# Kernel tuning notes

Hardware: AMD Instinct MI355X
Metric: run time of the kernel (lower is better)

The kernel has to match this reference:

```python
import jax, jax.numpy as jnp
import numpy as np

B, T, N, D, H, NMASK = 8192, 2, 40, 64, 1, 3
EPS = 1e-5


def setup_inputs() -> dict:
    key = jax.random.key(0)
    ks = jax.random.split(key, 12)
    F = T * N * 2 * D  # flattened feature size fed to BatchNorm1d
    return {
        "x": jax.random.normal(ks[0], (B, N, D), jnp.float32),
        "masker": jax.random.uniform(ks[1], (T, NMASK, N, N), jnp.float32, -0.27, 0.27),  # xavier-like
        "ln_gamma": jnp.ones((N,), jnp.float32),
        "ln_beta": jnp.zeros((N,), jnp.float32),
        "gnn_w": jax.random.normal(ks[2], (1, T, H, 2 * D, D), jnp.float32) * 0.05,
        "gnn_b": jax.random.normal(ks[3], (T, H, N, D), jnp.float32) * 0.05,
        "bn_gamma": jnp.ones((H, F), jnp.float32),
        "bn_beta": jnp.zeros((H, F), jnp.float32),
        "bn_mean": jax.random.normal(ks[4], (H, F), jnp.float32) * 0.1,
        "bn_var": jax.random.uniform(ks[5], (H, F), jnp.float32, 0.5, 1.5),
        "gate_w": jax.random.normal(ks[6], (N * D, N), jnp.float32) * 0.02,
        "gate_b": jnp.zeros((N,), jnp.float32),
    }


def reference(x, masker, ln_gamma, ln_beta, gnn_w, gnn_b, bn_gamma, bn_beta, bn_mean, bn_var, gate_w, gate_b):
    b = x.shape[0]
    # broadcast input to towers: (B, T, N, D)
    h = jnp.broadcast_to(x[:, None], (b, T, N, D))
    # adjacency from product of mask matrices: (T, N, N)
    adj = jax.nn.relu(jnp.prod(masker, axis=1))
    mask = (adj != 0).astype(x.dtype)
    # LayerNorm(num_fields) applied on transposed adj == normalize over rows (axis -2)
    mu = adj.mean(axis=-2, keepdims=True)
    var = adj.var(axis=-2, keepdims=True)
    ln = (adj - mu) / jnp.sqrt(var + EPS) * ln_gamma[:, None] + ln_beta[:, None]
    x_masked = ln + (1.0 - mask) * (-1e9) + jnp.eye(N, dtype=x.dtype)
    # softmax over rows (dim=1 of (T,N,N)) then re-mask
    A = jax.nn.softmax(x_masked, axis=1) * mask  # (T, N, N)
    for idx in range(H):
        # nei[b,t,n,d] = sum_m h[b,t,m,d] * A[t,m,n]
        nei = jnp.einsum('btmd,tmn->btnd', h, A)
        hc = jnp.concatenate([h, nei], axis=-1)  # (B,T,N,2D)
        flat = hc.reshape(b, -1)
        flat = (flat - bn_mean[idx]) / jnp.sqrt(bn_var[idx] + EPS) * bn_gamma[idx] + bn_beta[idx]
        hc = flat.reshape(b, T, N, 2 * D)
        # per-tower transform: (B,T,N,2D) x (T,2D,D) -> (B,T,N,D)
        h = jnp.einsum('btnf,tfd->btnd', hc, gnn_w[0, :, idx]) + gnn_b[:, idx]
    # attention pooling over fields
    logits = h.reshape(b, T, N * D) @ gate_w + gate_b  # (B,T,N)
    w = jax.nn.softmax(logits, axis=2)
    return jnp.sum(h * w[..., None], axis=2)  # (B, T, D)
```

## Files before the change

kernel.cpp:

```cpp
#include <hip/hip_runtime.h>
#include <hip/hip_bf16.h>
#include <stdint.h>

typedef float v4f __attribute__((ext_vector_type(4)));
typedef short v8s __attribute__((ext_vector_type(8)));
typedef union { v8s v; unsigned u[4]; } v8u;

#define NB 40
#define XSTR 42

__device__ __forceinline__ unsigned short f2b(float f) {
  __hip_bfloat16 h = __float2bfloat16(f);
  unsigned short u;
  __builtin_memcpy(&u, &h, 2);
  return u;
}
__device__ __forceinline__ unsigned pk2(float lo, float hi) {
  __hip_bfloat162 h = __float22bfloat162_rn(make_float2(lo, hi));
  unsigned u;
  __builtin_memcpy(&u, &h, 4);
  return u;
}
__device__ __forceinline__ float b2f16(unsigned short h) {
  return __uint_as_float(((unsigned)h) << 16);
}
__device__ __forceinline__ float blo(unsigned u) { return __uint_as_float(u << 16); }
__device__ __forceinline__ float bhi(unsigned u) { return __uint_as_float(u & 0xFFFF0000u); }


__global__ __launch_bounds__(256) void prep(
    const float* __restrict__ masker,
    const float* __restrict__ ln_gamma, const float* __restrict__ ln_beta,
    const float* __restrict__ gnn_w, const float* __restrict__ gnn_b,
    const float* __restrict__ bn_gamma, const float* __restrict__ bn_beta,
    const float* __restrict__ bn_mean, const float* __restrict__ bn_var,
    const float* __restrict__ gate_w,
    unsigned short* __restrict__ A1pk, unsigned short* __restrict__ W2pk,
    unsigned short* __restrict__ Gpk, float* __restrict__ s1,
    float* __restrict__ sNT, float* __restrict__ bias2T)
{
  const int tid = threadIdx.x;
  if (blockIdx.x == 0) {
    __shared__ float AtL[2 * NB * NB];
    const int w = tid >> 6, lane = tid & 63;
    #pragma unroll 1
    for (int it = 0; it < 20; ++it) {
      const int c = it * 4 + w;
      const int t = c / NB, n = c % NB;
      const int m = lane;
      float adj = 0.f;
      if (m < NB) {
        float p = masker[((t*3+0)*NB+m)*NB+n]
                * masker[((t*3+1)*NB+m)*NB+n]
                * masker[((t*3+2)*NB+m)*NB+n];
        adj = p > 0.f ? p : 0.f;
      }
      float s = adj;
      #pragma unroll
      for (int d = 1; d < 64; d <<= 1) s += __shfl_xor(s, d);
      const float mu = s * (1.f/NB);
      const float dv = (m < NB) ? adj - mu : 0.f;
      float v2 = dv * dv;
      #pragma unroll
      for (int d = 1; d < 64; d <<= 1) v2 += __shfl_xor(v2, d);
      const float inv = rsqrtf(v2 * (1.f/NB) + 1e-5f);
      float val = -3.0e38f;
      if (m < NB) {
        float lnv = dv * inv * ln_gamma[m] + ln_beta[m];
        val = lnv + (adj != 0.f ? 0.f : -1e9f) + (m == n ? 1.f : 0.f);
      }
      float mx = val;
      #pragma unroll
      for (int d = 1; d < 64; d <<= 1) mx = fmaxf(mx, __shfl_xor(mx, d));
      const float e = (m < NB) ? __expf(val - mx) : 0.f;
      float es = e;
      #pragma unroll
      for (int d = 1; d < 64; d <<= 1) es += __shfl_xor(es, d);
      if (m < NB)
        AtL[(t*NB+n)*NB + m] = (adj != 0.f) ? e / es : 0.f;
    }
    __syncthreads();
    for (int e = tid; e < 6144; e += 256) {
      int frag = e >> 9, rem = e & 511, lane2 = rem >> 3, jj = rem & 7;
      int t = frag / 6, r2 = frag % 6, nt = r2 >> 1, ks = r2 & 1;
      int n = nt*16 + (lane2 & 15);
      int m = ks*32 + (lane2 >> 4)*8 + jj;
      A1pk[e] = f2b((n < NB && m < NB) ? AtL[(t*NB+n)*NB+m] : 0.f);
    }
  } else {
    const int gid = (blockIdx.x - 1) * 256 + tid, gsz = 63 * 256;
    for (int e = gid; e < 16384; e += gsz) {
      int frag = e >> 9, rem = e & 511, lane = rem >> 3, jj = rem & 7;
      int t = frag >> 4, ks = (frag >> 2) & 3, dt = frag & 3;
      int f = ks*32 + (lane >> 4)*8 + jj, d = dt*16 + (lane & 15);
      W2pk[e] = f2b(gnn_w[t*8192 + f*64 + d]);
    }
    for (int e = gid; e < 122880; e += gsz) {
      int frag = e >> 9, rem = e & 511, lane = rem >> 3, jj = rem & 7;
      int kt = frag / 3, jt = frag % 3;
      int fl = kt*32 + (lane >> 4)*8 + jj, j = jt*16 + (lane & 15);
      Gpk[e] = f2b(j < NB ? gate_w[fl*NB + j] : 0.f);
    }
    for (int e = gid; e < 5120; e += gsz) {
      int t = e / 2560, n = (e % 2560) / 64, d = e & 63;
      int F = (t*NB + n)*128 + d;
      s1[e] = bn_gamma[F] * rsqrtf(bn_var[F] + 1e-5f);
    }
    for (int e = gid; e < 5120; e += gsz) {
      int t = e / 2560, d = (e % 2560) / 40, n = e % 40;
      int F = (t*NB + n)*128 + 64 + d;
      sNT[e] = bn_gamma[F] * rsqrtf(bn_var[F] + 1e-5f);
    }
    for (int e4 = gid; e4 < 20480; e4 += gsz) {
      int e = e4 >> 2, part = e4 & 3;
      int t = e / 2560, d = (e % 2560) / 40, n = e % 40;
      float acc = (part == 0) ? gnn_b[(t*NB + n)*64 + d] : 0.f;
      int Fb = (t*NB + n)*128;
      int f0 = part * 32;
      for (int f = f0; f < f0 + 32; ++f) {
        float s = bn_gamma[Fb+f] * rsqrtf(bn_var[Fb+f] + 1e-5f);
        float o = bn_beta[Fb+f] - bn_mean[Fb+f] * s;
        acc += o * gnn_w[t*8192 + f*64 + d];
      }
      acc += __shfl_xor(acc, 1);
      acc += __shfl_xor(acc, 2);
      if (part == 0) bias2T[e] = acc;
    }
  }
}

__global__ __launch_bounds__(256) void kernelM(
    const float* __restrict__ x,
    const unsigned short* __restrict__ A1pk, const unsigned short* __restrict__ W2pk,
    const unsigned short* __restrict__ Gpk, const float* __restrict__ s1,
    const float* __restrict__ sNT, const float* __restrict__ bias2T,
    const float* __restrict__ gate_b, float* __restrict__ out)
{
  __shared__ __align__(16) unsigned short hc[160 * 136];
  __shared__ float pj[16 * 48];

  const int tid = threadIdx.x;
  const int lane = tid & 63;
  const int w = tid >> 6;
  const int l = lane & 15, q = lane >> 4;
  const int t = blockIdx.x & 1;
  const int b0 = (blockIdx.x >> 1) * 4;
  unsigned* hcU = (unsigned*)hc;
  unsigned short* hL = hc;

  uint4 xr[5];
  #pragma unroll
  for (int it = 0; it < 5; ++it) {
    const int c = it * 256 + tid, row = c >> 3, dp8 = c & 7;
    const float* xp = x + (size_t)b0 * 2560 + row * 64 + dp8 * 8;
    const float4 f0 = *(const float4*)xp;
    const float4 f1 = *(const float4*)(xp + 4);
    xr[it] = make_uint4(pk2(f0.x, f0.y), pk2(f0.z, f0.w),
                        pk2(f1.x, f1.y), pk2(f1.z, f1.w));
  }
  for (int k = tid; k < 268; k += 256)
    hcU[(k < 256) ? (k * 21 + 20) : (5376 + (k - 256))] = 0u;
  #pragma unroll
  for (int it = 0; it < 5; ++it) {
    const int c = it * 256 + tid, row = c >> 3, dp8 = c & 7;
    const int bq = row / NB, n = row - bq * NB;
    unsigned short* base = hc + (bq * 64 + dp8 * 8) * XSTR + n;
    const unsigned uu0 = xr[it].x, uu1 = xr[it].y, uu2 = xr[it].z, uu3 = xr[it].w;
    base[0*XSTR] = (unsigned short)(uu0 & 0xFFFF);
    base[1*XSTR] = (unsigned short)(uu0 >> 16);
    base[2*XSTR] = (unsigned short)(uu1 & 0xFFFF);
    base[3*XSTR] = (unsigned short)(uu1 >> 16);
    base[4*XSTR] = (unsigned short)(uu2 & 0xFFFF);
    base[5*XSTR] = (unsigned short)(uu2 >> 16);
    base[6*XSTR] = (unsigned short)(uu3 & 0xFFFF);
    base[7*XSTR] = (unsigned short)(uu3 >> 16);
  }
  __syncthreads();
  v8s b1[4][2];
  #pragma unroll
  for (int i = 0; i < 4; ++i) {
    const int R = (w * 4 + i) * 16 + l;
    #pragma unroll
    for (int ks = 0; ks < 2; ++ks) {
      const unsigned* p = hcU + R * 21 + ks * 16 + q * 4;
      v8u uu;
      uu.u[0] = p[0]; uu.u[1] = p[1]; uu.u[2] = p[2]; uu.u[3] = p[3];
      b1[i][ks] = uu.v;
    }
  }
  __syncthreads();

  v8s a1[3][2], w2[4];
  #pragma unroll
  for (int nt = 0; nt < 3; ++nt)
    #pragma unroll
    for (int ks = 0; ks < 2; ++ks)
      a1[nt][ks] = *(const v8s*)(A1pk + (((t*3 + nt)*2 + ks) << 9) + lane*8);
  #pragma unroll
  for (int ks = 0; ks < 4; ++ks)
    w2[ks] = *(const v8s*)(W2pk + (((t*4 + ks)*4 + w) << 9) + lane*8);

  #pragma unroll
  for (int it = 0; it < 5; ++it) {
    const int c = it*256 + tid;
    const int row = c >> 3, dp8 = c & 7;
    const uint4 xv = xr[it];
    const int n = row % NB;
    const float4 sA = *(const float4*)(s1 + (t*NB + n)*64 + dp8*8);
    const float4 sB = *(const float4*)(s1 + (t*NB + n)*64 + dp8*8 + 4);
    uint4 p;
    p.x = pk2(blo(xv.x)*sA.x, bhi(xv.x)*sA.y);
    p.y = pk2(blo(xv.y)*sA.z, bhi(xv.y)*sA.w);
    p.z = pk2(blo(xv.z)*sB.x, bhi(xv.z)*sB.y);
    p.w = pk2(blo(xv.w)*sB.z, bhi(xv.w)*sB.w);
    *(uint4*)(hcU + row*68 + dp8*4) = p;
  }
  #pragma unroll
  for (int i = 0; i < 4; ++i) {
    const int R = (w*4+i)*16 + l;
    const int bb = R >> 6, d = R & 63;
    #pragma unroll
    for (int nt = 0; nt < 3; ++nt) {
      v4f acc = {0.f, 0.f, 0.f, 0.f};
      acc = __builtin_amdgcn_mfma_f32_16x16x32_bf16(a1[nt][0], b1[i][0], acc, 0, 0, 0);
      acc = __builtin_amdgcn_mfma_f32_16x16x32_bf16(a1[nt][1], b1[i][1], acc, 0, 0, 0);
      const float4 sv = *(const float4*)(sNT + (t*64+d)*40 + nt*16 + q*4);
      #pragma unroll
      for (int r = 0; r < 4; ++r) {
        int n = nt*16 + q*4 + r;
        if (n < NB) hc[(bb*NB + n)*136 + 64 + d] = f2b(acc[r]*sv[r]);
      }
    }
  }
  __syncthreads();
  unsigned pkr0[10], pkr1[10];
  #pragma unroll
  for (int mt = 0; mt < 10; ++mt) {
    v4f acc = {0.f, 0.f, 0.f, 0.f};
    #pragma unroll
    for (int ks = 0; ks < 4; ++ks) {
      v8s af = *(const v8s*)(hc + (mt*16 + l)*136 + ks*32 + q*8);
      acc = __builtin_amdgcn_mfma_f32_16x16x32_bf16(af, w2[ks], acc, 0, 0, 0);
    }
    const int d = w*16 + l;
    const int G = mt*16 + q*4;
    const int bb = G / NB, n0 = G - bb*NB;
    const float4 bv = *(const float4*)(bias2T + (t*64+d)*40 + n0);
    pkr0[mt] = pk2(acc[0] + bv.x, acc[1] + bv.y);
    pkr1[mt] = pk2(acc[2] + bv.z, acc[3] + bv.w);
  }
  __syncthreads();
  #pragma unroll
  for (int mt = 0; mt < 10; ++mt) {
    const int d = w*16 + l;
    const int G = mt*16 + q*4;
    const int bb = G / NB, n0 = G - bb*NB;
    hL[bb*2568 + (n0+0)*64 + d] = (unsigned short)(pkr0[mt] & 0xFFFF);
    hL[bb*2568 + (n0+1)*64 + d] = (unsigned short)(pkr0[mt] >> 16);
    hL[bb*2568 + (n0+2)*64 + d] = (unsigned short)(pkr1[mt] & 0xFFFF);
    hL[bb*2568 + (n0+3)*64 + d] = (unsigned short)(pkr1[mt] >> 16);
  }
  __syncthreads();
  v4f ac0 = {0,0,0,0}, ac1 = {0,0,0,0}, ac2 = {0,0,0,0};
  {
    v8s pg0[2], pg1[2], pg2[2], pbf[2];
    #pragma unroll
    for (int s = 0; s < 2; ++s) {
      const int kt = w + s*4;
      pg0[s] = *(const v8s*)(Gpk + ((kt*3+0) << 9) + lane*8);
      pg1[s] = *(const v8s*)(Gpk + ((kt*3+1) << 9) + lane*8);
      pg2[s] = *(const v8s*)(Gpk + ((kt*3+2) << 9) + lane*8);
      pbf[s] = *(const v8s*)(hL + (l & 3)*2568 + kt*32 + q*8);
    }
    #pragma unroll
    for (int i = 0; i < 20; ++i) {
      const int cur = i & 1;
      const v8s G0 = pg0[cur], G1 = pg1[cur], G2 = pg2[cur], BF = pbf[cur];
      if (i < 18) {
        const int ktn = w + (i+2)*4;
        pg0[cur] = *(const v8s*)(Gpk + ((ktn*3+0) << 9) + lane*8);
        pg1[cur] = *(const v8s*)(Gpk + ((ktn*3+1) << 9) + lane*8);
        pg2[cur] = *(const v8s*)(Gpk + ((ktn*3+2) << 9) + lane*8);
        pbf[cur] = *(const v8s*)(hL + (l & 3)*2568 + ktn*32 + q*8);
      }
      ac0 = __builtin_amdgcn_mfma_f32_16x16x32_bf16(G0, BF, ac0, 0, 0, 0);
      ac1 = __builtin_amdgcn_mfma_f32_16x16x32_bf16(G1, BF, ac1, 0, 0, 0);
      ac2 = __builtin_amdgcn_mfma_f32_16x16x32_bf16(G2, BF, ac2, 0, 0, 0);
    }
  }
  if (l < 4) {
    #pragma unroll
    for (int r = 0; r < 4; ++r) {
      pj[(w*4 + l)*48 +  0 + q*4 + r] = ac0[r];
      pj[(w*4 + l)*48 + 16 + q*4 + r] = ac1[r];
      pj[(w*4 + l)*48 + 32 + q*4 + r] = ac2[r];
    }
  }
  __syncthreads();
  {
    float v = -3.0e38f;
    if (lane < NB) {
      v = gate_b[lane];
      #pragma unroll
      for (int ww = 0; ww < 4; ++ww) v += pj[(ww*4 + w)*48 + lane];
    }
    float mx = v;
    #pragma unroll
    for (int m = 1; m < 64; m <<= 1) mx = fmaxf(mx, __shfl_xor(mx, m));
    float e = (lane < NB) ? __expf(v - mx) : 0.f;
    float es = e;
    #pragma unroll
    for (int m = 1; m < 64; m <<= 1) es += __shfl_xor(es, m);
    const float wgt = e / es;
    float accp = 0.f;
    #pragma unroll 8
    for (int n = 0; n < NB; ++n)
      accp += b2f16(hL[w*2568 + n*64 + lane]) * __shfl(wgt, n);
    out[((size_t)(b0 + w)*2 + t)*64 + lane] = accp;
  }
}

extern "C" void kernel_launch(void* const* d_in, const int* in_sizes, int n_in,
                              void* d_out, int out_size, void* d_ws, size_t ws_size,
                              hipStream_t stream) {
  const float* x        = (const float*)d_in[0];
  const float* masker   = (const float*)d_in[1];
  const float* ln_gamma = (const float*)d_in[2];
  const float* ln_beta  = (const float*)d_in[3];
  const float* gnn_w    = (const float*)d_in[4];
  const float* gnn_b    = (const float*)d_in[5];
  const float* bn_gamma = (const float*)d_in[6];
  const float* bn_beta  = (const float*)d_in[7];
  const float* bn_mean  = (const float*)d_in[8];
  const float* bn_var   = (const float*)d_in[9];
  const float* gate_w   = (const float*)d_in[10];
  const float* gate_b   = (const float*)d_in[11];
  float* out = (float*)d_out;

  char* ws = (char*)d_ws;
  unsigned short* A1pk   = (unsigned short*)(ws + 0);
  unsigned short* W2pk   = (unsigned short*)(ws + 12288);
  unsigned short* Gpk    = (unsigned short*)(ws + 45056);
  float*          s1     = (float*)(ws + 290816);
  float*          sNT    = (float*)(ws + 311296);
  float*          bias2T = (float*)(ws + 331904);

  prep<<<64, 256, 0, stream>>>(masker, ln_gamma, ln_beta, gnn_w, gnn_b,
                               bn_gamma, bn_beta, bn_mean, bn_var, gate_w,
                               A1pk, W2pk, Gpk, s1, sNT, bias2T);
  kernelM<<<4096, 256, 0, stream>>>(x, A1pk, W2pk, Gpk,
                                    s1, sNT, bias2T, gate_b, out);
}
```

Measured before the change: 235.6 us.

## Process eight batch rows per 512-thread block and split gate GEMM K across waves

Each block now handles 8 batch items with 8 waves instead of 4 items with 4 waves, halving the grid. The hL output tile gets its own shared buffer, which removes one barrier and the register staging of results. The gate projection's K loop is split across 8 waves, so each wave does 10 iterations and covers 8 batch rows per B fragment. The block ID mapping is also changed so that both towers of the same batch group land on nearby blocks for L2 reuse of x. Shared memory roughly doubles, which may lower occupancy.

```diff
diff --git a/kernel.cpp b/kernel.cpp
--- a/kernel.cpp
+++ b/kernel.cpp
@@ -129,40 +129,44 @@
   }
 }
 
-__global__ __launch_bounds__(256) void kernelM(
+__global__ __launch_bounds__(512) void kernelM(
     const float* __restrict__ x,
     const unsigned short* __restrict__ A1pk, const unsigned short* __restrict__ W2pk,
     const unsigned short* __restrict__ Gpk, const float* __restrict__ s1,
     const float* __restrict__ sNT, const float* __restrict__ bias2T,
     const float* __restrict__ gate_b, float* __restrict__ out)
 {
-  __shared__ __align__(16) unsigned short hc[160 * 136];
-  __shared__ float pj[16 * 48];
+  __shared__ __align__(16) unsigned short hc[320 * 136];
+  __shared__ __align__(16) unsigned short hL[8 * 2568];
+  __shared__ float pj[64 * 48];
 
   const int tid = threadIdx.x;
   const int lane = tid & 63;
   const int w = tid >> 6;
   const int l = lane & 15, q = lane >> 4;
-  const int t = blockIdx.x & 1;
-  const int b0 = (blockIdx.x >> 1) * 4;
+  const int bid = blockIdx.x;
+  const int t  = (bid >> 3) & 1;
+  const int bg = (bid & 7) | ((bid >> 4) << 3);
+  const int b0 = bg * 8;
   unsigned* hcU = (unsigned*)hc;
-  unsigned short* hL = hc;
+
+  const float* xblk = x + (size_t)b0 * 2560;
 
   uint4 xr[5];
   #pragma unroll
   for (int it = 0; it < 5; ++it) {
-    const int c = it * 256 + tid, row = c >> 3, dp8 = c & 7;
-    const float* xp = x + (size_t)b0 * 2560 + row * 64 + dp8 * 8;
+    const int c = it * 512 + tid, row = c >> 3, dp8 = c & 7;
+    const float* xp = xblk + row * 64 + dp8 * 8;
     const float4 f0 = *(const float4*)xp;
     const float4 f1 = *(const float4*)(xp + 4);
     xr[it] = make_uint4(pk2(f0.x, f0.y), pk2(f0.z, f0.w),
                         pk2(f1.x, f1.y), pk2(f1.z, f1.w));
   }
-  for (int k = tid; k < 268; k += 256)
-    hcU[(k < 256) ? (k * 21 + 20) : (5376 + (k - 256))] = 0u;
+  for (int k = tid; k < 528; k += 512)
+    hcU[(k < 512) ? (k * 21 + 20) : (10752 + (k - 512))] = 0u;
   #pragma unroll
   for (int it = 0; it < 5; ++it) {
-    const int c = it * 256 + tid, row = c >> 3, dp8 = c & 7;
+    const int c = it * 512 + tid, row = c >> 3, dp8 = c & 7;
     const int bq = row / NB, n = row - bq * NB;
     unsigned short* base = hc + (bq * 64 + dp8 * 8) * XSTR + n;
     const unsigned uu0 = xr[it].x, uu1 = xr[it].y, uu2 = xr[it].z, uu3 = xr[it].w;
@@ -198,11 +202,11 @@
       a1[nt][ks] = *(const v8s*)(A1pk + (((t*3 + nt)*2 + ks) << 9) + lane*8);
   #pragma unroll
   for (int ks = 0; ks < 4; ++ks)
-    w2[ks] = *(const v8s*)(W2pk + (((t*4 + ks)*4 + w) << 9) + lane*8);
+    w2[ks] = *(const v8s*)(W2pk + (((t*4 + ks)*4 + (w & 3)) << 9) + lane*8);
 
   #pragma unroll
   for (int it = 0; it < 5; ++it) {
-    const int c = it*256 + tid;
+    const int c = it*512 + tid;
     const int row = c >> 3, dp8 = c & 7;
     const uint4 xv = xr[it];
     const int n = row % NB;
@@ -233,67 +237,59 @@
     }
   }
   __syncthreads();
-  unsigned pkr0[10], pkr1[10];
-  #pragma unroll
-  for (int mt = 0; mt < 10; ++mt) {
+  #pragma unroll
+  for (int mj = 0; mj < 10; ++mj) {
+    const int mt = (w >> 2) * 10 + mj;
     v4f acc = {0.f, 0.f, 0.f, 0.f};
     #pragma unroll
     for (int ks = 0; ks < 4; ++ks) {
       v8s af = *(const v8s*)(hc + (mt*16 + l)*136 + ks*32 + q*8);
       acc = __builtin_amdgcn_mfma_f32_16x16x32_bf16(af, w2[ks], acc, 0, 0, 0);
     }
-    const int d = w*16 + l;
+    const int d = (w & 3)*16 + l;
     const int G = mt*16 + q*4;
     const int bb = G / NB, n0 = G - bb*NB;
     const float4 bv = *(const float4*)(bias2T + (t*64+d)*40 + n0);
-    pkr0[mt] = pk2(acc[0] + bv.x, acc[1] + bv.y);
-    pkr1[mt] = pk2(acc[2] + bv.z, acc[3] + bv.w);
-  }
-  __syncthreads();
-  #pragma unroll
-  for (int mt = 0; mt < 10; ++mt) {
-    const int d = w*16 + l;
-    const int G = mt*16 + q*4;
-    const int bb = G / NB, n0 = G - bb*NB;
-    hL[bb*2568 + (n0+0)*64 + d] = (unsigned short)(pkr0[mt] & 0xFFFF);
-    hL[bb*2568 + (n0+1)*64 + d] = (unsigned short)(pkr0[mt] >> 16);
-    hL[bb*2568 + (n0+2)*64 + d] = (unsigned short)(pkr1[mt] & 0xFFFF);
-    hL[bb*2568 + (n0+3)*64 + d] = (unsigned short)(pkr1[mt] >> 16);
+    hL[bb*2568 + (n0+0)*64 + d] = f2b(acc[0] + bv.x);
+    hL[bb*2568 + (n0+1)*64 + d] = f2b(acc[1] + bv.y);
+    hL[bb*2568 + (n0+2)*64 + d] = f2b(acc[2] + bv.z);
+    hL[bb*2568 + (n0+3)*64 + d] = f2b(acc[3] + bv.w);
   }
   __syncthreads();
   v4f ac0 = {0,0,0,0}, ac1 = {0,0,0,0}, ac2 = {0,0,0,0};
   {
+    const unsigned short* hb = hL + (l & 7)*2568 + q*8;
     v8s pg0[2], pg1[2], pg2[2], pbf[2];
     #pragma unroll
     for (int s = 0; s < 2; ++s) {
-      const int kt = w + s*4;
+      const int kt = w + s*8;
       pg0[s] = *(const v8s*)(Gpk + ((kt*3+0) << 9) + lane*8);
       pg1[s] = *(const v8s*)(Gpk + ((kt*3+1) << 9) + lane*8);
       pg2[s] = *(const v8s*)(Gpk + ((kt*3+2) << 9) + lane*8);
-      pbf[s] = *(const v8s*)(hL + (l & 3)*2568 + kt*32 + q*8);
-    }
-    #pragma unroll
-    for (int i = 0; i < 20; ++i) {
+      pbf[s] = *(const v8s*)(hb + kt*32);
+    }
+    #pragma unroll
+    for (int i = 0; i < 10; ++i) {
       const int cur = i & 1;
       const v8s G0 = pg0[cur], G1 = pg1[cur], G2 = pg2[cur], BF = pbf[cur];
-      if (i < 18) {
-        const int ktn = w + (i+2)*4;
+      if (i < 8) {
+        const int ktn = w + (i+2)*8;
         pg0[cur] = *(const v8s*)(Gpk + ((ktn*3+0) << 9) + lane*8);
         pg1[cur] = *(const v8s*)(Gpk + ((ktn*3+1) << 9) + lane*8);
         pg2[cur] = *(const v8s*)(Gpk + ((ktn*3+2) << 9) + lane*8);
-        pbf[cur] = *(const v8s*)(hL + (l & 3)*2568 + ktn*32 + q*8);
+        pbf[cur] = *(const v8s*)(hb + ktn*32);
       }
       ac0 = __builtin_amdgcn_mfma_f32_16x16x32_bf16(G0, BF, ac0, 0, 0, 0);
       ac1 = __builtin_amdgcn_mfma_f32_16x16x32_bf16(G1, BF, ac1, 0, 0, 0);
       ac2 = __builtin_amdgcn_mfma_f32_16x16x32_bf16(G2, BF, ac2, 0, 0, 0);
     }
   }
-  if (l < 4) {
+  if (l < 8) {
     #pragma unroll
     for (int r = 0; r < 4; ++r) {
-      pj[(w*4 + l)*48 +  0 + q*4 + r] = ac0[r];
-      pj[(w*4 + l)*48 + 16 + q*4 + r] = ac1[r];
-      pj[(w*4 + l)*48 + 32 + q*4 + r] = ac2[r];
+      pj[(w*8 + l)*48 +  0 + q*4 + r] = ac0[r];
+      pj[(w*8 + l)*48 + 16 + q*4 + r] = ac1[r];
+      pj[(w*8 + l)*48 + 32 + q*4 + r] = ac2[r];
     }
   }
   __syncthreads();
@@ -302,7 +298,7 @@
     if (lane < NB) {
       v = gate_b[lane];
       #pragma unroll
-      for (int ww = 0; ww < 4; ++ww) v += pj[(ww*4 + w)*48 + lane];
+      for (int ww = 0; ww < 8; ++ww) v += pj[(ww*8 + w)*48 + lane];
     }
     float mx = v;
     #pragma unroll
@@ -348,6 +344,6 @@
   prep<<<64, 256, 0, stream>>>(masker, ln_gamma, ln_beta, gnn_w, gnn_b,
                                bn_gamma, bn_beta, bn_mean, bn_var, gate_w,
                                A1pk, W2pk, Gpk, s1, sNT, bias2T);
-  kernelM<<<4096, 256, 0, stream>>>(x, A1pk, W2pk, Gpk,
+  kernelM<<<2048, 512, 0, stream>>>(x, A1pk, W2pk, Gpk,
                                     s1, sNT, bias2T, gate_b, out);
 }
```

Measured after the change: 242.4 us. 2.9% more time.
